# Optimization experiments

Measured on AMD Instinct MI355X. Metric: run time of the kernel, lower is better.

Reference implementation:

```python
import jax, jax.numpy as jnp
import numpy as np

LORA_SCALE = 0.5
LAYER_IDX = 0
NUM_ADAPTERS = 8

def setup_inputs() -> dict:
    key = jax.random.key(0)
    ks = jax.random.split(key, 11)
    T, H, I, A, L, R = 2048, 4096, 11008, NUM_ADAPTERS, 1, 16
    s_base = 1.0 / np.sqrt(H)
    s_down = 1.0 / np.sqrt(I)
    return {
        "x": jax.random.normal(ks[0], (T, H), jnp.float32),
        "gate_w": jax.random.normal(ks[1], (I, H), jnp.float32) * s_base,
        "up_w": jax.random.normal(ks[2], (I, H), jnp.float32) * s_base,
        "down_w": jax.random.normal(ks[3], (H, I), jnp.float32) * s_down,
        "gate_wa": jax.random.normal(ks[4], (A, L, R, H), jnp.float32) * s_base,
        "gate_wb": jax.random.normal(ks[5], (A, L, I, R), jnp.float32) * 0.01,
        "up_wa": jax.random.normal(ks[6], (A, L, R, H), jnp.float32) * s_base,
        "up_wb": jax.random.normal(ks[7], (A, L, I, R), jnp.float32) * 0.01,
        "down_wa": jax.random.normal(ks[8], (A, L, R, I), jnp.float32) * s_down,
        "down_wb": jax.random.normal(ks[9], (A, L, H, R), jnp.float32) * 0.01,
        "indices": jax.random.randint(ks[10], (T,), 0, A, jnp.int64),
    }

def _add_lora(y, x_in, wa, wb, idx, scale):
    # wa: [A, L, r, in], wb: [A, L, out, r]; per-token adapter gather (BGMV)
    wa_t = wa[idx, LAYER_IDX]          # [T, r, in]
    wb_t = wb[idx, LAYER_IDX]          # [T, out, r]
    v = jnp.einsum('ti,tri->tr', x_in, wa_t)     # [T, r]
    return y + scale * jnp.einsum('tr,tor->to', v, wb_t)

def reference(x, gate_w, up_w, down_w, gate_wa, gate_wb, up_wa, up_wb, down_wa, down_wb, indices):
    gate = x @ gate_w.T                                   # [T, I]
    gate = _add_lora(gate, x, gate_wa, gate_wb, indices, LORA_SCALE)
    gate = jax.nn.silu(gate)
    up = x @ up_w.T                                       # [T, I]
    up = _add_lora(up, x, up_wa, up_wb, indices, LORA_SCALE)
    t = gate * up                                         # [T, I]
    down = t @ down_w.T                                   # [T, H]
    down = _add_lora(down, t, down_wa, down_wb, indices, LORA_SCALE)
    return down
```

## Files before the change

### kernel.cpp

```cpp
#include <hip/hip_runtime.h>
#include <hip/hip_bf16.h>
#include <cstdint>


#define T_TOK 2048
#define H_DIM 4096
#define I_DIM 11008
#define R_LORA 16
#define KA1 4352
#define KA2 11136
#define N_STK 22016

typedef __bf16 bf16x8 __attribute__((ext_vector_type(8)));
typedef float f32x4 __attribute__((ext_vector_type(4)));

__device__ __forceinline__ float bf2f(unsigned short u) {
    union { unsigned int i; float f; } v;
    v.i = ((unsigned int)u) << 16;
    return v.f;
}
__device__ __forceinline__ unsigned short f2bf(float f) {
    __bf16 b = (__bf16)f;
    unsigned short u;
    __builtin_memcpy(&u, &b, 2);
    return u;
}
__device__ __forceinline__ void cvt8(const float* s, unsigned short* d) {
    float4 a = reinterpret_cast<const float4*>(s)[0];
    float4 b = reinterpret_cast<const float4*>(s)[1];
    uint4 o;
    o.x = (unsigned)f2bf(a.x) | ((unsigned)f2bf(a.y) << 16);
    o.y = (unsigned)f2bf(a.z) | ((unsigned)f2bf(a.w) << 16);
    o.z = (unsigned)f2bf(b.x) | ((unsigned)f2bf(b.y) << 16);
    o.w = (unsigned)f2bf(b.z) | ((unsigned)f2bf(b.w) << 16);
    *reinterpret_cast<uint4*>(d) = o;
}
__device__ __forceinline__ void gload_lds16(const void* g, void* l) {
    __builtin_amdgcn_global_load_lds(
        (const __attribute__((address_space(1))) void*)g,
        (__attribute__((address_space(3))) void*)l,
        16, 0, 0);
}

__global__ __launch_bounds__(256) void cvt_wa_all(
    const float* __restrict__ gwa, const float* __restrict__ uwa,
    const float* __restrict__ dwa,
    unsigned short* __restrict__ wab_gu, unsigned short* __restrict__ wab_d)
{
    const int row = blockIdx.x;
    const int tid = threadIdx.x;
    if (row < 256) {
        const float* s = (row < 128 ? gwa + (size_t)row * H_DIM
                                    : uwa + (size_t)(row - 128) * H_DIM);
        unsigned short* d = wab_gu + (size_t)row * H_DIM;
        for (int k = tid * 8; k < H_DIM; k += 2048) cvt8(s + k, d + k);
    } else {
        const int r = row - 256;
        const float* s = dwa + (size_t)r * I_DIM;
        unsigned short* d = wab_d + (size_t)r * I_DIM;
        for (int k = tid * 8; k < I_DIM; k += 2048) cvt8(s + k, d + k);
    }
}

__global__ __launch_bounds__(256) void build_xa_x(
    const float* __restrict__ x, unsigned short* __restrict__ xa)
{
    const int t = blockIdx.x;
    const int tid = threadIdx.x;
    const float* s = x + (size_t)t * H_DIM;
    unsigned short* d = xa + (size_t)t * KA1;
    for (int k = tid * 8; k < H_DIM; k += 2048) cvt8(s + k, d + k);
}

__global__ __launch_bounds__(256) void fill_xa_aug(
    const float* __restrict__ P, const int* __restrict__ idx,
    unsigned short* __restrict__ xa)
{
    const int t = blockIdx.x;
    const int tid = threadIdx.x;
    const int a = (tid & 127) >> 4;
    float v = 0.f;
    if (a == idx[t]) {
        #pragma unroll
        for (int s = 0; s < 4; ++s)
            v += P[((size_t)s * T_TOK + t) * 256 + tid];
        v *= 0.5f;
    }
    xa[(size_t)t * KA1 + H_DIM + tid] = f2bf(v);
}

__global__ __launch_bounds__(128) void fill_ta(
    const float* __restrict__ P, const int* __restrict__ idx,
    unsigned short* __restrict__ t_aug)
{
    const int t = blockIdx.x;
    const int tid = threadIdx.x;
    const int a = tid >> 4;
    float v = 0.f;
    if (a == idx[t]) {
        #pragma unroll
        for (int s = 0; s < 4; ++s)
            v += P[((size_t)s * T_TOK + t) * 128 + tid];
        v *= 0.5f;
    }
    t_aug[(size_t)t * KA2 + I_DIM + tid] = f2bf(v);
}

__global__ __launch_bounds__(256) void build_w_int(
    const float* __restrict__ gw, const float* __restrict__ uw,
    const float* __restrict__ gwb, const float* __restrict__ uwb,
    unsigned short* __restrict__ dst)
{
    const int c = blockIdx.x;
    const int i = c >> 1;
    const int par = c & 1;
    const int tid = threadIdx.x;
    const float* src = (par ? uw : gw) + (size_t)i * H_DIM;
    const float* wb  = (par ? uwb : gwb);
    unsigned short* d = dst + (size_t)c * KA1;
    for (int k = tid * 8; k < H_DIM; k += 256 * 8) cvt8(src + k, d + k);
    if (tid < 128) {
        const int a = tid >> 4, r = tid & 15;
        const float v = wb[(((size_t)a * I_DIM) + i) * R_LORA + r];
        d[H_DIM + par * 128 + tid] = f2bf(v);
        d[H_DIM + (1 - par) * 128 + tid] = 0;
    }
}

__global__ __launch_bounds__(256) void build_w_aug(
    const float* __restrict__ w, const float* __restrict__ wb,
    unsigned short* __restrict__ dst,
    int Nrows, int Ksrc, int Kdst, int self_off)
{
    const int c = blockIdx.x;
    const int tid = threadIdx.x;
    const float* src = w + (size_t)c * Ksrc;
    unsigned short* d = dst + (size_t)c * Kdst;
    for (int k = tid * 8; k < Ksrc; k += 256 * 8) cvt8(src + k, d + k);
    if (tid < 128) {
        const int a = tid >> 4, r = tid & 15;
        const float v = wb[(((size_t)a * Nrows) + c) * R_LORA + r];
        d[self_off + tid] = f2bf(v);
    }
}

__global__ __launch_bounds__(256) void add_inplace(
    float* __restrict__ out, const float* __restrict__ p)
{
    const long long n4 = (long long)T_TOK * H_DIM / 4;
    long long i = (long long)blockIdx.x * 256 + threadIdx.x;
    const long long stride = (long long)gridDim.x * 256;
    for (; i < n4; i += stride) {
        float4 a = reinterpret_cast<float4*>(out)[i];
        float4 b = reinterpret_cast<const float4*>(p)[i];
        a.x += b.x; a.y += b.y; a.z += b.z; a.w += b.w;
        reinterpret_cast<float4*>(out)[i] = a;
    }
}

__global__ __launch_bounds__(512) void gemm_thin_sk(
    const unsigned short* __restrict__ A, int lda,
    const unsigned short* __restrict__ B, int ldb,
    float* __restrict__ P, int N, int K)
{
    __shared__ __align__(16) unsigned short As[128][64];
    __shared__ __align__(16) unsigned short Bs[128][64];

    const int tid = threadIdx.x;
    const int lane = tid & 63;
    const int wid = tid >> 6;
    const int wr = wid >> 2;
    const int wc = wid & 3;
    const int fr = lane & 15;
    const int hi = lane >> 4;
    const int fsw = fr & 7;

    const int bm0 = blockIdx.y * 128;
    const int bn0 = blockIdx.x * 128;
    const int ks = K / 4;
    const int k0 = blockIdx.z * ks;
    float* out = P + (size_t)blockIdx.z * T_TOK * N;

    const int srow = tid >> 3;
    const int sslot = tid & 7;
    const int gcol = (sslot ^ (srow & 7)) * 8;
    const unsigned short* Ag = A + (size_t)(bm0 + srow) * lda + gcol;
    const unsigned short* Bg = B + (size_t)(bn0 + srow) * ldb + gcol;
    const size_t halfA = (size_t)64 * lda;
    const size_t halfB = (size_t)64 * ldb;

    f32x4 acc[4][2] = {};

    for (int kt = k0; kt < k0 + ks; kt += 64) {
        gload_lds16(Ag + kt,         &As[srow][sslot * 8]);
        gload_lds16(Ag + halfA + kt, &As[64 + srow][sslot * 8]);
        gload_lds16(Bg + kt,         &Bs[srow][sslot * 8]);
        gload_lds16(Bg + halfB + kt, &Bs[64 + srow][sslot * 8]);
        __syncthreads();
        #pragma unroll
        for (int kk = 0; kk < 2; ++kk) {
            bf16x8 a_[4], b_[2];
            #pragma unroll
            for (int m = 0; m < 4; ++m)
                a_[m] = *reinterpret_cast<const bf16x8*>(
                    &As[wr * 64 + m * 16 + fr][((kk * 4 + hi) ^ fsw) * 8]);
            #pragma unroll
            for (int n = 0; n < 2; ++n)
                b_[n] = *reinterpret_cast<const bf16x8*>(
                    &Bs[wc * 32 + n * 16 + fr][((kk * 4 + hi) ^ fsw) * 8]);
            #pragma unroll
            for (int m = 0; m < 4; ++m)
                #pragma unroll
                for (int n = 0; n < 2; ++n)
                    acc[m][n] = __builtin_amdgcn_mfma_f32_16x16x32_bf16(
                        a_[m], b_[n], acc[m][n], 0, 0, 0);
        }
        __syncthreads();
    }

    const int orow0 = bm0 + wr * 64 + hi * 4;
    const int ocol0 = bn0 + wc * 32 + fr;
    #pragma unroll
    for (int m = 0; m < 4; ++m)
        #pragma unroll
        for (int j = 0; j < 4; ++j) {
            const int row = orow0 + m * 16 + j;
            #pragma unroll
            for (int n = 0; n < 2; ++n)
                out[(size_t)row * N + ocol0 + n * 16] = acc[m][n][j];
        }
}

#define RD_A(BUF, MH)                                                         \
    do {                                                                      \
        _Pragma("unroll")                                                     \
        for (int mq = 0; mq < 4; ++mq) {                                      \
            _Pragma("unroll")                                                 \
            for (int k = 0; k < 2; ++k)                                       \
                a_[mq][k] = *reinterpret_cast<const bf16x8*>(                 \
                    &lds[BUF][wr * 128 + (MH) * 64 + mq * 16 + fr]            \
                        [((k * 4 + hi) ^ fsw) * 8]);                          \
        }                                                                     \
    } while (0)

#define RD_B(BUF, NH, DST)                                                    \
    do {                                                                      \
        _Pragma("unroll")                                                     \
        for (int nq = 0; nq < 2; ++nq) {                                      \
            _Pragma("unroll")                                                 \
            for (int k = 0; k < 2; ++k)                                       \
                DST[nq][k] = *reinterpret_cast<const bf16x8*>(                \
                    &lds[BUF][256 + wc * 64 + (NH) * 32 + nq * 16 + fr]       \
                        [((k * 4 + hi) ^ fsw) * 8]);                          \
        }                                                                     \
    } while (0)

#define MM(MH, NH, BSRC)                                                      \
    do {                                                                      \
        _Pragma("unroll")                                                     \
        for (int mq = 0; mq < 4; ++mq) {                                      \
            _Pragma("unroll")                                                 \
            for (int nq = 0; nq < 2; ++nq) {                                  \
                _Pragma("unroll")                                             \
                for (int k = 0; k < 2; ++k)                                   \
                    acc[(MH) * 4 + mq][(NH) * 2 + nq] =                       \
                        __builtin_amdgcn_mfma_f32_16x16x32_bf16(              \
                            a_[mq][k], BSRC[nq][k],                           \
                            acc[(MH) * 4 + mq][(NH) * 2 + nq], 0, 0, 0);      \
            }                                                                 \
        }                                                                     \
    } while (0)

template <int MODE>
__global__ __launch_bounds__(512, 2) void gemmk(
    const unsigned short* __restrict__ A, int lda,
    const unsigned short* __restrict__ B, int ldb,
    int nks_in,
    unsigned short* __restrict__ outb,
    float* __restrict__ outf0, float* __restrict__ outf1)
{
    __shared__ __align__(16) unsigned short lds[2][512][64];

    const int tid = threadIdx.x;
    const int lane = tid & 63;
    const int wid = tid >> 6;
    const int wr = wid >> 2;
    const int wc = wid & 3;
    const int fr = lane & 15;
    const int hi = lane >> 4;
    const int fsw = fr & 7;

    int bm, bn, koff = 0, nks = nks_in;
    float* outf = outf0;
    if constexpr (MODE == 2) {
        const int xcd = blockIdx.x & 7;
        const int c = blockIdx.x >> 3;
        bm = (xcd >> 1) * 2 + (c & 1);
        bn = (xcd & 1) * 8 + ((c >> 1) & 7);
        nks = 87;
        if (c >> 4) { koff = 87 * 64; outf = outf1; }
    } else {
        bm = blockIdx.x & 7;
        bn = blockIdx.x >> 3;
    }
    const int bm0 = bm * 256;
    const int bn0 = bn * 256;

    const int srow = tid >> 3;
    const int sslot = tid & 7;
    const int gcol = (sslot ^ (srow & 7)) * 8;
    const unsigned short* Ap = A + (size_t)(bm0 + srow) * lda + gcol + koff;
    const unsigned short* Bp = B + (size_t)(bn0 + srow) * ldb + gcol + koff;

    f32x4 acc[8][4] = {};
    bf16x8 a_[4][2], b0_[2][2], b1_[2][2];

    auto stage = [&](int buf, int kt) {
        #pragma unroll
        for (int q = 0; q < 4; ++q)
            gload_lds16(Ap + (size_t)(q * 64) * lda + kt,
                        &lds[buf][q * 64 + srow][sslot * 8]);
        #pragma unroll
        for (int q = 0; q < 4; ++q)
            gload_lds16(Bp + (size_t)(q * 64) * ldb + kt,
                        &lds[buf][256 + q * 64 + srow][sslot * 8]);
    };

    stage(0, 0);
    __syncthreads();

    for (int t = 0; t < nks; ++t) {
        const int cur = t & 1;
        if (t + 1 < nks) stage(cur ^ 1, (t + 1) * 64);

        RD_A(cur, 0);
        RD_B(cur, 0, b0_);
        MM(0, 0, b0_);
        RD_B(cur, 1, b1_);
        MM(0, 1, b1_);
        RD_A(cur, 1);
        MM(1, 0, b0_);
        MM(1, 1, b1_);

        __syncthreads();
    }

    const int orow0 = bm0 + wr * 128 + hi * 4;
    const int ocol0 = bn0 + wc * 64 + fr;
    #pragma unroll
    for (int m = 0; m < 8; ++m) {
        #pragma unroll
        for (int jj = 0; jj < 4; ++jj) {
            const int row = orow0 + m * 16 + jj;
            #pragma unroll
            for (int n = 0; n < 4; ++n) {
                if constexpr (MODE == 3) {
                    const float v = acc[m][n][jj];
                    const float w = __shfl_xor(v, 1);
                    if ((fr & 1) == 0) {
                        const float sg = v / (1.f + __expf(-v));
                        const int s = ocol0 + n * 16;
                        outb[(size_t)row * KA2 + (s >> 1)] = f2bf(sg * w);
                    }
                } else {
                    outf[(size_t)row * H_DIM + ocol0 + n * 16] = acc[m][n][jj];
                }
            }
        }
    }
}

extern "C" void kernel_launch(void* const* d_in, const int* in_sizes, int n_in,
                              void* d_out, int out_size, void* d_ws, size_t ws_size,
                              hipStream_t stream)
{
    const float* x       = (const float*)d_in[0];
    const float* gate_w  = (const float*)d_in[1];
    const float* up_w    = (const float*)d_in[2];
    const float* down_w  = (const float*)d_in[3];
    const float* gate_wa = (const float*)d_in[4];
    const float* gate_wb = (const float*)d_in[5];
    const float* up_wa   = (const float*)d_in[6];
    const float* up_wb   = (const float*)d_in[7];
    const float* down_wa = (const float*)d_in[8];
    const float* down_wb = (const float*)d_in[9];
    const int*   indices = (const int*)d_in[10];
    float* out = (float*)d_out;

    char* ws = (char*)d_ws;
    size_t off = 0;
    auto alloc = [&](size_t bytes) {
        char* p = ws + off;
        off += (bytes + 255) & ~(size_t)255;
        return p;
    };
    unsigned short* xa     = (unsigned short*)alloc((size_t)T_TOK * KA1 * 2);
    unsigned short* wB     = (unsigned short*)alloc((size_t)N_STK * KA1 * 2);
    unsigned short* t_aug  = (unsigned short*)alloc((size_t)T_TOK * KA2 * 2);
    unsigned short* wab_gu = (unsigned short*)alloc((size_t)256 * H_DIM * 2);
    unsigned short* wab_d  = (unsigned short*)alloc((size_t)128 * I_DIM * 2);
    float* partial1        = (float*)alloc((size_t)T_TOK * H_DIM * 4);

    float* Pgu = (float*)t_aug;
    float* Pd  = (float*)xa;
    unsigned short* wd_aug = wB;

    cvt_wa_all<<<384, 256, 0, stream>>>(gate_wa, up_wa, down_wa, wab_gu, wab_d);
    build_xa_x<<<T_TOK, 256, 0, stream>>>(x, xa);
    gemm_thin_sk<<<dim3(2, 16, 4), 512, 0, stream>>>(xa, KA1, wab_gu, H_DIM, Pgu, 256, H_DIM);
    fill_xa_aug<<<T_TOK, 256, 0, stream>>>(Pgu, indices, xa);

    build_w_int<<<N_STK, 256, 0, stream>>>(gate_w, up_w, gate_wb, up_wb, wB);

    gemmk<3><<<8 * (N_STK / 256), 512, 0, stream>>>(
        xa, KA1, wB, KA1, KA1 / 64, t_aug, nullptr, nullptr);

    gemm_thin_sk<<<dim3(1, 16, 4), 512, 0, stream>>>(t_aug, KA2, wab_d, I_DIM, Pd, 128, I_DIM);
    fill_ta<<<T_TOK, 128, 0, stream>>>(Pd, indices, t_aug);
    build_w_aug<<<H_DIM, 256, 0, stream>>>(down_w, down_wb, wd_aug,
                                           H_DIM, I_DIM, KA2, I_DIM);

    gemmk<2><<<256, 512, 0, stream>>>(
        t_aug, KA2, wd_aug, KA2, 0, nullptr, out, partial1);
    add_inplace<<<2048, 256, 0, stream>>>(out, partial1);

    (void)in_sizes; (void)n_in; (void)out_size; (void)ws_size;
}
```

Baseline: 805.6 us.

## Make gate/up GEMM persistent over N tiles and merge prep kernels

```diff
diff --git a/kernel.cpp b/kernel.cpp
--- a/kernel.cpp
+++ b/kernel.cpp
@@ -42,34 +42,30 @@
         16, 0, 0);
 }
 
-__global__ __launch_bounds__(256) void cvt_wa_all(
+__global__ __launch_bounds__(256) void prep_all(
+    const float* __restrict__ x, unsigned short* __restrict__ xa,
     const float* __restrict__ gwa, const float* __restrict__ uwa,
     const float* __restrict__ dwa,
     unsigned short* __restrict__ wab_gu, unsigned short* __restrict__ wab_d)
 {
     const int row = blockIdx.x;
     const int tid = threadIdx.x;
-    if (row < 256) {
-        const float* s = (row < 128 ? gwa + (size_t)row * H_DIM
-                                    : uwa + (size_t)(row - 128) * H_DIM);
-        unsigned short* d = wab_gu + (size_t)row * H_DIM;
+    if (row < 2048) {
+        const float* s = x + (size_t)row * H_DIM;
+        unsigned short* d = xa + (size_t)row * KA1;
+        for (int k = tid * 8; k < H_DIM; k += 2048) cvt8(s + k, d + k);
+    } else if (row < 2304) {
+        const int r = row - 2048;
+        const float* s = (r < 128 ? gwa + (size_t)r * H_DIM
+                                  : uwa + (size_t)(r - 128) * H_DIM);
+        unsigned short* d = wab_gu + (size_t)r * H_DIM;
         for (int k = tid * 8; k < H_DIM; k += 2048) cvt8(s + k, d + k);
     } else {
-        const int r = row - 256;
+        const int r = row - 2304;
         const float* s = dwa + (size_t)r * I_DIM;
         unsigned short* d = wab_d + (size_t)r * I_DIM;
         for (int k = tid * 8; k < I_DIM; k += 2048) cvt8(s + k, d + k);
     }
-}
-
-__global__ __launch_bounds__(256) void build_xa_x(
-    const float* __restrict__ x, unsigned short* __restrict__ xa)
-{
-    const int t = blockIdx.x;
-    const int tid = threadIdx.x;
-    const float* s = x + (size_t)t * H_DIM;
-    unsigned short* d = xa + (size_t)t * KA1;
-    for (int k = tid * 8; k < H_DIM; k += 2048) cvt8(s + k, d + k);
 }
 
 __global__ __launch_bounds__(256) void fill_xa_aug(
@@ -289,81 +285,86 @@
     const int fr = lane & 15;
     const int hi = lane >> 4;
     const int fsw = fr & 7;
-
-    int bm, bn, koff = 0, nks = nks_in;
+    const int srow = tid >> 3;
+    const int sslot = tid & 7;
+    const int gcol = (sslot ^ (srow & 7)) * 8;
+
+    int bm, bn0_tile, ntiles, koff = 0, nks = nks_in;
     float* outf = outf0;
     if constexpr (MODE == 2) {
         const int xcd = blockIdx.x & 7;
         const int c = blockIdx.x >> 3;
         bm = (xcd >> 1) * 2 + (c & 1);
-        bn = (xcd & 1) * 8 + ((c >> 1) & 7);
+        bn0_tile = (xcd & 1) * 8 + ((c >> 1) & 7);
+        ntiles = 1;
         nks = 87;
         if (c >> 4) { koff = 87 * 64; outf = outf1; }
     } else {
         bm = blockIdx.x & 7;
-        bn = blockIdx.x >> 3;
+        const int local = blockIdx.x >> 3;
+        if (local < 22) { ntiles = 3; bn0_tile = local * 3; }
+        else            { ntiles = 2; bn0_tile = 66 + (local - 22) * 2; }
     }
     const int bm0 = bm * 256;
-    const int bn0 = bn * 256;
-
-    const int srow = tid >> 3;
-    const int sslot = tid & 7;
-    const int gcol = (sslot ^ (srow & 7)) * 8;
     const unsigned short* Ap = A + (size_t)(bm0 + srow) * lda + gcol + koff;
-    const unsigned short* Bp = B + (size_t)(bn0 + srow) * ldb + gcol + koff;
-
-    f32x4 acc[8][4] = {};
-    bf16x8 a_[4][2], b0_[2][2], b1_[2][2];
-
-    auto stage = [&](int buf, int kt) {
+
+    for (int ti = 0; ti < ntiles; ++ti) {
+        const int bn0 = (bn0_tile + ti) * 256;
+        const unsigned short* Bp = B + (size_t)(bn0 + srow) * ldb + gcol + koff;
+
+        f32x4 acc[8][4] = {};
+        bf16x8 a_[4][2], b0_[2][2], b1_[2][2];
+
+        auto stage = [&](int buf, int kt) {
+            #pragma unroll
+            for (int q = 0; q < 4; ++q)
+                gload_lds16(Ap + (size_t)(q * 64) * lda + kt,
+                            &lds[buf][q * 64 + srow][sslot * 8]);
+            #pragma unroll
+            for (int q = 0; q < 4; ++q)
+                gload_lds16(Bp + (size_t)(q * 64) * ldb + kt,
+                            &lds[buf][256 + q * 64 + srow][sslot * 8]);
+        };
+
+        stage(0, 0);
+        __syncthreads();
+
+        for (int t = 0; t < nks; ++t) {
+            const int cur = t & 1;
+            if (t + 1 < nks) stage(cur ^ 1, (t + 1) * 64);
+
+            RD_A(cur, 0);
+            RD_B(cur, 0, b0_);
+            MM(0, 0, b0_);
+            RD_B(cur, 1, b1_);
+            MM(0, 1, b1_);
+            RD_A(cur, 1);
+            MM(1, 0, b0_);
+            MM(1, 1, b1_);
+
+            __syncthreads();
+        }
+
+        const int orow0 = bm0 + wr * 128 + hi * 4;
+        const int ocol0 = bn0 + wc * 64 + fr;
         #pragma unroll
-        for (int q = 0; q < 4; ++q)
-            gload_lds16(Ap + (size_t)(q * 64) * lda + kt,
-                        &lds[buf][q * 64 + srow][sslot * 8]);
-        #pragma unroll
-        for (int q = 0; q < 4; ++q)
-            gload_lds16(Bp + (size_t)(q * 64) * ldb + kt,
-                        &lds[buf][256 + q * 64 + srow][sslot * 8]);
-    };
-
-    stage(0, 0);
-    __syncthreads();
-
-    for (int t = 0; t < nks; ++t) {
-        const int cur = t & 1;
-        if (t + 1 < nks) stage(cur ^ 1, (t + 1) * 64);
-
-        RD_A(cur, 0);
-        RD_B(cur, 0, b0_);
-        MM(0, 0, b0_);
-        RD_B(cur, 1, b1_);
-        MM(0, 1, b1_);
-        RD_A(cur, 1);
-        MM(1, 0, b0_);
-        MM(1, 1, b1_);
-
-        __syncthreads();
-    }
-
-    const int orow0 = bm0 + wr * 128 + hi * 4;
-    const int ocol0 = bn0 + wc * 64 + fr;
-    #pragma unroll
-    for (int m = 0; m < 8; ++m) {
-        #pragma unroll
-        for (int jj = 0; jj < 4; ++jj) {
-            const int row = orow0 + m * 16 + jj;
-            #pragma unroll
-            for (int n = 0; n < 4; ++n) {
-                if constexpr (MODE == 3) {
-                    const float v = acc[m][n][jj];
-                    const float w = __shfl_xor(v, 1);
-                    if ((fr & 1) == 0) {
-                        const float sg = v / (1.f + __expf(-v));
-                        const int s = ocol0 + n * 16;
-                        outb[(size_t)row * KA2 + (s >> 1)] = f2bf(sg * w);
+        for (int m = 0; m < 8; ++m) {
+            #pragma unroll
+            for (int jj = 0; jj < 4; ++jj) {
+                const int row = orow0 + m * 16 + jj;
+                #pragma unroll
+                for (int n = 0; n < 4; ++n) {
+                    if constexpr (MODE == 3) {
+                        const float v = acc[m][n][jj];
+                        const float w = __shfl_xor(v, 1);
+                        if ((fr & 1) == 0) {
+                            const float sg = v / (1.f + __expf(-v));
+                            const int s = ocol0 + n * 16;
+                            outb[(size_t)row * KA2 + (s >> 1)] = f2bf(sg * w);
+                        }
+                    } else {
+                        outf[(size_t)row * H_DIM + ocol0 + n * 16] = acc[m][n][jj];
                     }
-                } else {
-                    outf[(size_t)row * H_DIM + ocol0 + n * 16] = acc[m][n][jj];
                 }
             }
         }
@@ -405,14 +406,13 @@
     float* Pd  = (float*)xa;
     unsigned short* wd_aug = wB;
 
-    cvt_wa_all<<<384, 256, 0, stream>>>(gate_wa, up_wa, down_wa, wab_gu, wab_d);
-    build_xa_x<<<T_TOK, 256, 0, stream>>>(x, xa);
+    prep_all<<<2432, 256, 0, stream>>>(x, xa, gate_wa, up_wa, down_wa, wab_gu, wab_d);
     gemm_thin_sk<<<dim3(2, 16, 4), 512, 0, stream>>>(xa, KA1, wab_gu, H_DIM, Pgu, 256, H_DIM);
     fill_xa_aug<<<T_TOK, 256, 0, stream>>>(Pgu, indices, xa);
 
     build_w_int<<<N_STK, 256, 0, stream>>>(gate_w, up_w, gate_wb, up_wb, wB);
 
-    gemmk<3><<<8 * (N_STK / 256), 512, 0, stream>>>(
+    gemmk<3><<<256, 512, 0, stream>>>(
         xa, KA1, wB, KA1, KA1 / 64, t_aug, nullptr, nullptr);
 
     gemm_thin_sk<<<dim3(1, 16, 4), 512, 0, stream>>>(t_aug, KA2, wab_d, I_DIM, Pd, 128, I_DIM);
```

After: 806.2 us. Within noise of the previous version (+0.1%).
